# Performance work log

Measured on AMD Instinct MI355X. Metric: run time of the kernel, lower is better.

## Reference

```python
import jax, jax.numpy as jnp
import numpy as np

INPUT_DIM = 1024
EMBED_DIMS = 128


def setup_inputs() -> dict:
    key = jax.random.key(0)
    ks = jax.random.split(key, 7)
    s_in = 1.0 / np.sqrt(INPUT_DIM)
    x = jax.random.normal(ks[0], (4, 4096, INPUT_DIM), dtype=jnp.float32)
    Wq = jax.random.uniform(ks[1], (INPUT_DIM, EMBED_DIMS), jnp.float32, -s_in, s_in)
    bq = jax.random.uniform(ks[2], (EMBED_DIMS,), jnp.float32, -s_in, s_in)
    Wk = jax.random.uniform(ks[3], (INPUT_DIM, EMBED_DIMS), jnp.float32, -s_in, s_in)
    bk = jax.random.uniform(ks[4], (EMBED_DIMS,), jnp.float32, -s_in, s_in)
    Wv = jax.random.uniform(ks[5], (INPUT_DIM, EMBED_DIMS), jnp.float32, -s_in, s_in)
    bv = jax.random.uniform(ks[6], (EMBED_DIMS,), jnp.float32, -s_in, s_in)
    return {"x": x, "Wq": Wq, "bq": bq, "Wk": Wk, "bk": bk, "Wv": Wv, "bv": bv}


def reference(x, Wq, bq, Wk, bk, Wv, bv):
    # x: [B, L, C]
    Q = jnp.einsum('blc,cd->bld', x, Wq) + bq  # [B, L, D]
    K = jnp.einsum('blc,cd->bld', x, Wk) + bk
    V = jnp.einsum('blc,cd->bld', x, Wv) + bv
    d_k = Q.shape[-1]
    scores = jnp.einsum('bld,bmd->blm', Q, K) / jnp.sqrt(jnp.float32(d_k))  # [B, L, L]
    attn = jax.nn.softmax(scores, axis=-1)
    return jnp.einsum('blm,bmd->bld', attn, V)  # [B, L, D]
```

## Files before the change

### kernel.cpp

```cpp
#include <hip/hip_runtime.h>
#include <stdint.h>

typedef __bf16 bf16;
typedef __bf16 bf16x8 __attribute__((ext_vector_type(8)));
typedef __bf16 bf16x4 __attribute__((ext_vector_type(4)));
typedef _Float16 f16;
typedef f16 f16x8 __attribute__((ext_vector_type(8)));
typedef f16 f16x4 __attribute__((ext_vector_type(4)));
typedef float f32x16 __attribute__((ext_vector_type(16)));
typedef uint32_t u32x4 __attribute__((ext_vector_type(4)));

#define LQ    16384
#define CDIM  1024
#define DDIM  128
#define NSPLIT 4
#define QS 0.12751741f

static __device__ __forceinline__ uint32_t pkrtz(float a, float b) {
  return __builtin_bit_cast(uint32_t, __builtin_amdgcn_cvt_pkrtz(a, b));
}

static __device__ __forceinline__ void lds_barrier() {
  asm volatile("s_waitcnt lgkmcnt(0)" ::: "memory");
  __builtin_amdgcn_s_barrier();
}

static __device__ __forceinline__ void gload_lds16(const void* g, void* l) {
  __builtin_amdgcn_global_load_lds(
      (__attribute__((address_space(1))) void*)g,
      (__attribute__((address_space(3))) void*)l, 16, 0, 0);
}

__global__ void prep_kernel(const float* __restrict__ Wq, const float* __restrict__ Wk,
                            const float* __restrict__ Wv, const float* __restrict__ bq,
                            const float* __restrict__ bk, const float* __restrict__ bv,
                            bf16* __restrict__ Wt, float* __restrict__ bias_all) {
  int idx = blockIdx.x * 256 + threadIdx.x;
  int p = idx >> 17;
  int rem = idx & 131071;
  int k = rem >> 7, n = rem & 127;
  const float* W = (p == 0) ? Wq : (p == 1) ? Wk : Wv;
  float s = (p == 0) ? QS : 1.0f;
  Wt[(size_t)(p * 128 + n) * CDIM + k] = (bf16)(W[rem] * s);
  if (idx < 384) {
    int pp = idx >> 7, nn = idx & 127;
    const float* b = (pp == 0) ? bq : (pp == 1) ? bk : bv;
    bias_all[idx] = b[nn] * ((pp == 0) ? QS : 1.0f);
  }
}

__global__ __launch_bounds__(512, 1) void qkv_gemm(
    const float* __restrict__ x, const bf16* __restrict__ Wt,
    const float* __restrict__ bias_all,
    bf16* __restrict__ Qw, bf16* __restrict__ Kw, f16* __restrict__ Vtw) {
  __shared__ bf16 As[2][64 * 64];
  __shared__ bf16 Bs[2][384 * 64];
  const int t = threadIdx.x;
  const int w = t >> 6;
  const int lane = t & 63;
  const int l31 = lane & 31;
  const int hi = lane >> 5;
  const int m0 = blockIdx.x * 64;
  const int m_off = (w & 1) * 32;
  const int n_off = ((w >> 1) & 3) * 32;

  const f32x16 z16 = {0.f,0.f,0.f,0.f,0.f,0.f,0.f,0.f,0.f,0.f,0.f,0.f,0.f,0.f,0.f,0.f};
  f32x16 acc[3];
  acc[0] = z16; acc[1] = z16; acc[2] = z16;

  const int srow = t >> 3;
  const int g = t & 7;
  const int sgoff = (g ^ (srow & 7)) * 8;
  const int scol = g * 8;

  const int lrow = lane >> 3;
  const int lgr = (lane & 7) ^ lrow;
  const bf16* bsrc = Wt + (size_t)(w * 48 + lrow) * CDIM + lgr * 8;

  float4 xc0, xc1, xn0, xn1;

#pragma unroll
  for (int c = 0; c < 6; c++)
    gload_lds16(bsrc + (size_t)c * 8 * CDIM, &Bs[0][(w * 48 + c * 8) * 64]);
  {
    const float* p = &x[(size_t)(m0 + srow) * CDIM + scol];
    float4 a0 = *(const float4*)p;
    float4 a1 = *(const float4*)(p + 4);
    bf16x8 v;
    v[0] = (bf16)a0.x; v[1] = (bf16)a0.y; v[2] = (bf16)a0.z; v[3] = (bf16)a0.w;
    v[4] = (bf16)a1.x; v[5] = (bf16)a1.y; v[6] = (bf16)a1.z; v[7] = (bf16)a1.w;
    *(bf16x8*)&As[0][srow * 64 + sgoff] = v;
  }
  {
    const float* p = &x[(size_t)(m0 + srow) * CDIM + 64 + scol];
    xc0 = *(const float4*)p;
    xc1 = *(const float4*)(p + 4);
  }
  lds_barrier();

  for (int kc = 0; kc < 16; kc++) {
    bf16* Ab = As[kc & 1];
    bf16* Bb = Bs[kc & 1];

    if (kc < 15) {
      const bf16* s = bsrc + (kc + 1) * 64;
      bf16* Bn = Bs[(kc + 1) & 1];
#pragma unroll
      for (int c = 0; c < 6; c++)
        gload_lds16(s + (size_t)c * 8 * CDIM, &Bn[(w * 48 + c * 8) * 64]);
      __builtin_amdgcn_sched_barrier(0);
      if (kc < 14) {
        const float* p = &x[(size_t)(m0 + srow) * CDIM + (kc + 2) * 64 + scol];
        xn0 = *(const float4*)p;
        xn1 = *(const float4*)(p + 4);
      }
    }

#pragma unroll
    for (int ks = 0; ks < 4; ks++) {
      const int rg = ((ks * 2 + hi) ^ (l31 & 7)) * 8;
      bf16x8 af = *(const bf16x8*)&Ab[(m_off + l31) * 64 + rg];
#pragma unroll
      for (int p = 0; p < 3; p++) {
        bf16x8 bfr = *(const bf16x8*)&Bb[(p * 128 + n_off + l31) * 64 + rg];
        acc[p] = __builtin_amdgcn_mfma_f32_32x32x16_bf16(af, bfr, acc[p], 0, 0, 0);
      }
    }

    if (kc < 15) {
      bf16* An = As[(kc + 1) & 1];
      bf16x8 v;
      v[0] = (bf16)xc0.x; v[1] = (bf16)xc0.y; v[2] = (bf16)xc0.z; v[3] = (bf16)xc0.w;
      v[4] = (bf16)xc1.x; v[5] = (bf16)xc1.y; v[6] = (bf16)xc1.z; v[7] = (bf16)xc1.w;
      *(bf16x8*)&An[srow * 64 + sgoff] = v;
      __builtin_amdgcn_sched_barrier(0);
      if (kc < 14)
        asm volatile("s_waitcnt vmcnt(2)" ::: "memory");
      else
        asm volatile("s_waitcnt vmcnt(0)" ::: "memory");
      lds_barrier();
      xc0 = xn0; xc1 = xn1;
    }
  }

  const int n = n_off + l31;
#pragma unroll
  for (int p = 0; p < 3; p++) {
    const float bias = bias_all[p * 128 + n];
    if (p < 2) {
      bf16* outp = (p == 0) ? Qw : Kw;
#pragma unroll
      for (int r = 0; r < 16; r++) {
        int m = m0 + m_off + (r & 3) + 8 * (r >> 2) + 4 * hi;
        outp[(size_t)m * DDIM + n] = (bf16)(acc[p][r] + bias);
      }
    } else {
#pragma unroll
      for (int gq = 0; gq < 4; gq++) {
        int mbase = m0 + m_off + 8 * gq + 4 * hi;
        f16x4 pv;
#pragma unroll
        for (int r = 0; r < 4; r++) pv[r] = (f16)(acc[p][gq * 4 + r] + bias);
        *(f16x4*)&Vtw[(size_t)n * LQ + mbase] = pv;
      }
    }
  }
}

__global__ __launch_bounds__(256, 2) void flash_kernel(
    const bf16* __restrict__ Qw, const bf16* __restrict__ Kw, const f16* __restrict__ Vtw,
    bf16* __restrict__ Opb, float* __restrict__ lp) {
  __shared__ bf16 Kl[2][64 * 136];
  __shared__ f16  Vl[2][128 * 72];

  const int t = threadIdx.x;
  const int w = t >> 6;
  const int lane = t & 63;
  const int l31 = lane & 31;
  const int hi = lane >> 5;
  const int lin = blockIdx.y * 128 + blockIdx.x;
  const int logical = ((lin & 7) << 6) + (lin >> 3);
  const int qb = logical & 127;
  const int sp = logical >> 7;
  const int batch = qb >> 5;
  const int q0w = qb * 128 + w * 32;
  const int kv_base = batch * 4096 + sp * 1024;

  bf16x8 qf[8];
#pragma unroll
  for (int ks = 0; ks < 8; ks++)
    qf[ks] = *(const bf16x8*)&Qw[(size_t)(q0w + l31) * DDIM + ks * 16 + hi * 8];

  const f32x16 z16 = {0.f,0.f,0.f,0.f,0.f,0.f,0.f,0.f,0.f,0.f,0.f,0.f,0.f,0.f,0.f,0.f};
  f32x16 o[4];
  o[0] = z16; o[1] = z16; o[2] = z16; o[3] = z16;
  f32x16 liacc = z16;

  f16x8 ones;
#pragma unroll
  for (int i = 0; i < 8; i++) ones[i] = (f16)1.f;

  const int kr = t >> 4;
  const int kcol = (t & 15) << 3;
  const int vr = t >> 3;
  const int vcol = (t & 7) << 3;

  bf16x8 ka[4];
  f16x8 va[4];
  f16x8 pa[4];

#pragma unroll
  for (int c = 0; c < 4; c++)
    ka[c] = *(const bf16x8*)&Kw[(size_t)(kv_base + c * 16 + kr) * DDIM + kcol];
#pragma unroll
  for (int c = 0; c < 4; c++)
    va[c] = *(const f16x8*)&Vtw[(size_t)(c * 32 + vr) * LQ + kv_base + vcol];

#pragma unroll
  for (int c = 0; c < 4; c++)
    *(bf16x8*)&Kl[0][(c * 16 + kr) * 136 + kcol] = ka[c];
#pragma unroll
  for (int c = 0; c < 4; c++)
    *(f16x8*)&Vl[0][(c * 32 + vr) * 72 + vcol] = va[c];

#pragma unroll
  for (int c = 0; c < 4; c++)
    ka[c] = *(const bf16x8*)&Kw[(size_t)(kv_base + 64 + c * 16 + kr) * DDIM + kcol];
#pragma unroll
  for (int c = 0; c < 4; c++)
    va[c] = *(const f16x8*)&Vtw[(size_t)(c * 32 + vr) * LQ + kv_base + 64 + vcol];

  lds_barrier();

  f32x16 sv0 = z16, sv1 = z16;
  __builtin_amdgcn_s_setprio(1);
#pragma unroll
  for (int ks = 0; ks < 8; ks++) {
    bf16x8 kf0 = *(const bf16x8*)&Kl[0][l31 * 136 + ks * 16 + hi * 8];
    bf16x8 kf1 = *(const bf16x8*)&Kl[0][(32 + l31) * 136 + ks * 16 + hi * 8];
    sv0 = __builtin_amdgcn_mfma_f32_32x32x16_bf16(kf0, qf[ks], sv0, 0, 0, 0);
    sv1 = __builtin_amdgcn_mfma_f32_32x32x16_bf16(kf1, qf[ks], sv1, 0, 0, 0);
  }
  __builtin_amdgcn_s_setprio(0);
#pragma unroll
  for (int r = 0; r < 16; r++) {
    sv0[r] = __builtin_amdgcn_exp2f(sv0[r]);
    sv1[r] = __builtin_amdgcn_exp2f(sv1[r]);
  }
#pragma unroll
  for (int sl = 0; sl < 4; sl++) {
    const int b = (sl & 1) * 8;
    float s0 = (sl >> 1) ? sv1[b + 0] : sv0[b + 0];
    float s1 = (sl >> 1) ? sv1[b + 1] : sv0[b + 1];
    float s2 = (sl >> 1) ? sv1[b + 2] : sv0[b + 2];
    float s3 = (sl >> 1) ? sv1[b + 3] : sv0[b + 3];
    float s4 = (sl >> 1) ? sv1[b + 4] : sv0[b + 4];
    float s5 = (sl >> 1) ? sv1[b + 5] : sv0[b + 5];
    float s6 = (sl >> 1) ? sv1[b + 6] : sv0[b + 6];
    float s7 = (sl >> 1) ? sv1[b + 7] : sv0[b + 7];
    uint32_t a0 = pkrtz(s0, s1);
    uint32_t a1 = pkrtz(s2, s3);
    uint32_t a2 = pkrtz(s4, s5);
    uint32_t a3 = pkrtz(s6, s7);
    asm("v_permlane32_swap_b32 %0, %1" : "+v"(a0), "+v"(a2));
    asm("v_permlane32_swap_b32 %0, %1" : "+v"(a1), "+v"(a3));
    u32x4 aw; aw.x = a0; aw.y = a1; aw.z = a2; aw.w = a3;
    pa[sl] = __builtin_bit_cast(f16x8, aw);
  }

  for (int tile = 0; tile < 15; tile++) {
    bf16* Kb = Kl[(tile + 1) & 1];
    f16*  Vb = Vl[(tile + 1) & 1];
    f16*  Vp = Vl[tile & 1];
#pragma unroll
    for (int c = 0; c < 4; c++)
      *(bf16x8*)&Kb[(c * 16 + kr) * 136 + kcol] = ka[c];
#pragma unroll
    for (int c = 0; c < 4; c++)
      *(f16x8*)&Vb[(c * 32 + vr) * 72 + vcol] = va[c];

    const int kvn = kv_base + (tile < 14 ? tile + 2 : 15) * 64;
#pragma unroll
    for (int c = 0; c < 4; c++)
      ka[c] = *(const bf16x8*)&Kw[(size_t)(kvn + c * 16 + kr) * DDIM + kcol];
#pragma unroll
    for (int c = 0; c < 4; c++)
      va[c] = *(const f16x8*)&Vtw[(size_t)(c * 32 + vr) * LQ + kvn + vcol];

    lds_barrier();

    sv0 = z16; sv1 = z16;
    __builtin_amdgcn_s_setprio(1);
#pragma unroll
    for (int i = 0; i < 4; i++) {
      bf16x8 kf0a = *(const bf16x8*)&Kb[l31 * 136 + (2 * i) * 16 + hi * 8];
      bf16x8 kf1a = *(const bf16x8*)&Kb[(32 + l31) * 136 + (2 * i) * 16 + hi * 8];
      bf16x8 kf0b = *(const bf16x8*)&Kb[l31 * 136 + (2 * i + 1) * 16 + hi * 8];
      bf16x8 kf1b = *(const bf16x8*)&Kb[(32 + l31) * 136 + (2 * i + 1) * 16 + hi * 8];
      sv0 = __builtin_amdgcn_mfma_f32_32x32x16_bf16(kf0a, qf[2 * i], sv0, 0, 0, 0);
      sv1 = __builtin_amdgcn_mfma_f32_32x32x16_bf16(kf1a, qf[2 * i], sv1, 0, 0, 0);
      const int koff = (i >> 1) * 32 + (i & 1) * 16 + hi * 8;
#pragma unroll
      for (int dt = 0; dt < 4; dt++) {
        f16x8 vf = *(const f16x8*)&Vp[(dt * 32 + l31) * 72 + koff];
        o[dt] = __builtin_amdgcn_mfma_f32_32x32x16_f16(pa[i], vf, o[dt], 0, 0, 0);
      }
      liacc = __builtin_amdgcn_mfma_f32_32x32x16_f16(pa[i], ones, liacc, 0, 0, 0);
      sv0 = __builtin_amdgcn_mfma_f32_32x32x16_bf16(kf0b, qf[2 * i + 1], sv0, 0, 0, 0);
      sv1 = __builtin_amdgcn_mfma_f32_32x32x16_bf16(kf1b, qf[2 * i + 1], sv1, 0, 0, 0);
    }
    __builtin_amdgcn_s_setprio(0);

#pragma unroll
    for (int r = 0; r < 16; r++) {
      sv0[r] = __builtin_amdgcn_exp2f(sv0[r]);
      sv1[r] = __builtin_amdgcn_exp2f(sv1[r]);
    }
#pragma unroll
    for (int sl = 0; sl < 4; sl++) {
      const int b = (sl & 1) * 8;
      float s0 = (sl >> 1) ? sv1[b + 0] : sv0[b + 0];
      float s1 = (sl >> 1) ? sv1[b + 1] : sv0[b + 1];
      float s2 = (sl >> 1) ? sv1[b + 2] : sv0[b + 2];
      float s3 = (sl >> 1) ? sv1[b + 3] : sv0[b + 3];
      float s4 = (sl >> 1) ? sv1[b + 4] : sv0[b + 4];
      float s5 = (sl >> 1) ? sv1[b + 5] : sv0[b + 5];
      float s6 = (sl >> 1) ? sv1[b + 6] : sv0[b + 6];
      float s7 = (sl >> 1) ? sv1[b + 7] : sv0[b + 7];
      uint32_t a0 = pkrtz(s0, s1);
      uint32_t a1 = pkrtz(s2, s3);
      uint32_t a2 = pkrtz(s4, s5);
      uint32_t a3 = pkrtz(s6, s7);
      asm("v_permlane32_swap_b32 %0, %1" : "+v"(a0), "+v"(a2));
      asm("v_permlane32_swap_b32 %0, %1" : "+v"(a1), "+v"(a3));
      u32x4 aw; aw.x = a0; aw.y = a1; aw.z = a2; aw.w = a3;
      pa[sl] = __builtin_bit_cast(f16x8, aw);
    }

    __builtin_amdgcn_s_barrier();
  }

  {
    f16* Vp = Vl[15 & 1];
    __builtin_amdgcn_s_setprio(1);
#pragma unroll
    for (int i = 0; i < 4; i++) {
      const int koff = (i >> 1) * 32 + (i & 1) * 16 + hi * 8;
#pragma unroll
      for (int dt = 0; dt < 4; dt++) {
        f16x8 vf = *(const f16x8*)&Vp[(dt * 32 + l31) * 72 + koff];
        o[dt] = __builtin_amdgcn_mfma_f32_32x32x16_f16(pa[i], vf, o[dt], 0, 0, 0);
      }
      liacc = __builtin_amdgcn_mfma_f32_32x32x16_f16(pa[i], ones, liacc, 0, 0, 0);
    }
    __builtin_amdgcn_s_setprio(0);
  }

  const size_t po = (size_t)sp * LQ * DDIM;
#pragma unroll
  for (int dt = 0; dt < 4; dt++)
#pragma unroll
    for (int r = 0; r < 16; r++) {
      int q = q0w + (r & 3) + 8 * (r >> 2) + 4 * hi;
      Opb[po + (size_t)q * DDIM + dt * 32 + l31] = (bf16)o[dt][r];
    }
  if (l31 == 0) {
#pragma unroll
    for (int r = 0; r < 16; r++)
      lp[(size_t)sp * LQ + q0w + (r & 3) + 8 * (r >> 2) + 4 * hi] = liacc[r];
  }
}

__global__ void combine_kernel(const bf16* __restrict__ Opb, const float* __restrict__ lp,
                               float* __restrict__ out) {
  int idx = blockIdx.x * 256 + threadIdx.x;
  int q = idx >> 5;
  int d = (idx & 31) * 4;
  float lsum = 0.f;
  float acc[4] = {0.f, 0.f, 0.f, 0.f};
#pragma unroll
  for (int sp = 0; sp < NSPLIT; sp++) {
    lsum += lp[(size_t)sp * LQ + q];
    bf16x4 ov = *(const bf16x4*)&Opb[(size_t)sp * LQ * DDIM + (size_t)q * DDIM + d];
#pragma unroll
    for (int j = 0; j < 4; j++) acc[j] += (float)ov[j];
  }
  float inv = 1.0f / lsum;
  float4 r;
  r.x = acc[0] * inv; r.y = acc[1] * inv; r.z = acc[2] * inv; r.w = acc[3] * inv;
  *(float4*)&out[(size_t)q * DDIM + d] = r;
}

extern "C" void kernel_launch(void* const* d_in, const int* in_sizes, int n_in,
                              void* d_out, int out_size, void* d_ws, size_t ws_size,
                              hipStream_t stream) {
  const float* x  = (const float*)d_in[0];
  const float* Wq = (const float*)d_in[1];
  const float* bq = (const float*)d_in[2];
  const float* Wk = (const float*)d_in[3];
  const float* bk = (const float*)d_in[4];
  const float* Wv = (const float*)d_in[5];
  const float* bv = (const float*)d_in[6];
  char* ws = (char*)d_ws;
  bf16* Qw   = (bf16*)(ws);
  bf16* Kw   = (bf16*)(ws + ((size_t)4 << 20));
  f16*  Vtw  = (f16*)(ws + ((size_t)8 << 20));
  bf16* Wt   = (bf16*)(ws + ((size_t)12 << 20));
  float* bias_all = (float*)(ws + ((size_t)12 << 20) + 786432);
  bf16* Opb  = (bf16*)(ws + ((size_t)13 << 20));
  float* lpp = (float*)(ws + ((size_t)29 << 20));
  float* out = (float*)d_out;

  prep_kernel<<<1536, 256, 0, stream>>>(Wq, Wk, Wv, bq, bk, bv, Wt, bias_all);
  qkv_gemm<<<256, 512, 0, stream>>>(x, Wt, bias_all, Qw, Kw, Vtw);
  flash_kernel<<<dim3(128, NSPLIT), 256, 0, stream>>>(Qw, Kw, Vtw, Opb, lpp);
  combine_kernel<<<2048, 256, 0, stream>>>(Opb, lpp, out);
}
```

Measured before the change: 167.3 us.

## Process 64 query rows per wave in flash kernel to reuse K/V fragments

Each wave now handles two 32-row query tiles instead of one. Every K and V fragment read from LDS therefore feeds twice as many MFMAs, and the grid shrinks from 512 to 256 blocks, each covering 256 queries. Launch bounds drop to one block per SIMD-set to leave room for the doubled accumulators. The cost is much higher register pressure and lower occupancy, with 256 blocks on a 256-CU device giving only one wave of blocks and less latency hiding.

```diff
diff --git a/kernel.cpp b/kernel.cpp
--- a/kernel.cpp
+++ b/kernel.cpp
@@ -167,7 +167,7 @@
   }
 }
 
-__global__ __launch_bounds__(256, 2) void flash_kernel(
+__global__ __launch_bounds__(256, 1) void flash_kernel(
     const bf16* __restrict__ Qw, const bf16* __restrict__ Kw, const f16* __restrict__ Vtw,
     bf16* __restrict__ Opb, float* __restrict__ lp) {
   __shared__ bf16 Kl[2][64 * 136];
@@ -178,23 +178,26 @@
   const int lane = t & 63;
   const int l31 = lane & 31;
   const int hi = lane >> 5;
-  const int lin = blockIdx.y * 128 + blockIdx.x;
-  const int logical = ((lin & 7) << 6) + (lin >> 3);
-  const int qb = logical & 127;
-  const int sp = logical >> 7;
-  const int batch = qb >> 5;
-  const int q0w = qb * 128 + w * 32;
+  const int lin = blockIdx.y * 64 + blockIdx.x;
+  const int logical = ((lin & 7) << 5) + (lin >> 3);
+  const int qb = logical & 63;
+  const int sp = logical >> 6;
+  const int batch = qb >> 4;
+  const int q0w = qb * 256 + w * 64;
   const int kv_base = batch * 4096 + sp * 1024;
 
-  bf16x8 qf[8];
-#pragma unroll
-  for (int ks = 0; ks < 8; ks++)
-    qf[ks] = *(const bf16x8*)&Qw[(size_t)(q0w + l31) * DDIM + ks * 16 + hi * 8];
+  bf16x8 qf0[8], qf1[8];
+#pragma unroll
+  for (int ks = 0; ks < 8; ks++) {
+    qf0[ks] = *(const bf16x8*)&Qw[(size_t)(q0w + l31) * DDIM + ks * 16 + hi * 8];
+    qf1[ks] = *(const bf16x8*)&Qw[(size_t)(q0w + 32 + l31) * DDIM + ks * 16 + hi * 8];
+  }
 
   const f32x16 z16 = {0.f,0.f,0.f,0.f,0.f,0.f,0.f,0.f,0.f,0.f,0.f,0.f,0.f,0.f,0.f,0.f};
-  f32x16 o[4];
-  o[0] = z16; o[1] = z16; o[2] = z16; o[3] = z16;
-  f32x16 liacc = z16;
+  f32x16 o0[4], o1[4];
+#pragma unroll
+  for (int dt = 0; dt < 4; dt++) { o0[dt] = z16; o1[dt] = z16; }
+  f32x16 li0 = z16, li1 = z16;
 
   f16x8 ones;
 #pragma unroll
@@ -207,7 +210,7 @@
 
   bf16x8 ka[4];
   f16x8 va[4];
-  f16x8 pa[4];
+  f16x8 pa0[4], pa1[4];
 
 #pragma unroll
   for (int c = 0; c < 4; c++)
@@ -232,40 +235,50 @@
 
   lds_barrier();
 
-  f32x16 sv0 = z16, sv1 = z16;
+  f32x16 s00 = z16, s01 = z16, s10 = z16, s11 = z16;
   __builtin_amdgcn_s_setprio(1);
 #pragma unroll
   for (int ks = 0; ks < 8; ks++) {
     bf16x8 kf0 = *(const bf16x8*)&Kl[0][l31 * 136 + ks * 16 + hi * 8];
     bf16x8 kf1 = *(const bf16x8*)&Kl[0][(32 + l31) * 136 + ks * 16 + hi * 8];
-    sv0 = __builtin_amdgcn_mfma_f32_32x32x16_bf16(kf0, qf[ks], sv0, 0, 0, 0);
-    sv1 = __builtin_amdgcn_mfma_f32_32x32x16_bf16(kf1, qf[ks], sv1, 0, 0, 0);
+    s00 = __builtin_amdgcn_mfma_f32_32x32x16_bf16(kf0, qf0[ks], s00, 0, 0, 0);
+    s01 = __builtin_amdgcn_mfma_f32_32x32x16_bf16(kf0, qf1[ks], s01, 0, 0, 0);
+    s10 = __builtin_amdgcn_mfma_f32_32x32x16_bf16(kf1, qf0[ks], s10, 0, 0, 0);
+    s11 = __builtin_amdgcn_mfma_f32_32x32x16_bf16(kf1, qf1[ks], s11, 0, 0, 0);
   }
   __builtin_amdgcn_s_setprio(0);
 #pragma unroll
   for (int r = 0; r < 16; r++) {
-    sv0[r] = __builtin_amdgcn_exp2f(sv0[r]);
-    sv1[r] = __builtin_amdgcn_exp2f(sv1[r]);
+    s00[r] = __builtin_amdgcn_exp2f(s00[r]);
+    s01[r] = __builtin_amdgcn_exp2f(s01[r]);
+    s10[r] = __builtin_amdgcn_exp2f(s10[r]);
+    s11[r] = __builtin_amdgcn_exp2f(s11[r]);
   }
 #pragma unroll
   for (int sl = 0; sl < 4; sl++) {
     const int b = (sl & 1) * 8;
-    float s0 = (sl >> 1) ? sv1[b + 0] : sv0[b + 0];
-    float s1 = (sl >> 1) ? sv1[b + 1] : sv0[b + 1];
-    float s2 = (sl >> 1) ? sv1[b + 2] : sv0[b + 2];
-    float s3 = (sl >> 1) ? sv1[b + 3] : sv0[b + 3];
-    float s4 = (sl >> 1) ? sv1[b + 4] : sv0[b + 4];
-    float s5 = (sl >> 1) ? sv1[b + 5] : sv0[b + 5];
-    float s6 = (sl >> 1) ? sv1[b + 6] : sv0[b + 6];
-    float s7 = (sl >> 1) ? sv1[b + 7] : sv0[b + 7];
-    uint32_t a0 = pkrtz(s0, s1);
-    uint32_t a1 = pkrtz(s2, s3);
-    uint32_t a2 = pkrtz(s4, s5);
-    uint32_t a3 = pkrtz(s6, s7);
-    asm("v_permlane32_swap_b32 %0, %1" : "+v"(a0), "+v"(a2));
-    asm("v_permlane32_swap_b32 %0, %1" : "+v"(a1), "+v"(a3));
-    u32x4 aw; aw.x = a0; aw.y = a1; aw.z = a2; aw.w = a3;
-    pa[sl] = __builtin_bit_cast(f16x8, aw);
+    {
+      const f32x16 s = (sl >> 1) ? s10 : s00;
+      uint32_t a0 = pkrtz(s[b + 0], s[b + 1]);
+      uint32_t a1 = pkrtz(s[b + 2], s[b + 3]);
+      uint32_t a2 = pkrtz(s[b + 4], s[b + 5]);
+      uint32_t a3 = pkrtz(s[b + 6], s[b + 7]);
+      asm("v_permlane32_swap_b32 %0, %1" : "+v"(a0), "+v"(a2));
+      asm("v_permlane32_swap_b32 %0, %1" : "+v"(a1), "+v"(a3));
+      u32x4 aw; aw.x = a0; aw.y = a1; aw.z = a2; aw.w = a3;
+      pa0[sl] = __builtin_bit_cast(f16x8, aw);
+    }
+    {
+      const f32x16 s = (sl >> 1) ? s11 : s01;
+      uint32_t a0 = pkrtz(s[b + 0], s[b + 1]);
+      uint32_t a1 = pkrtz(s[b + 2], s[b + 3]);
+      uint32_t a2 = pkrtz(s[b + 4], s[b + 5]);
+      uint32_t a3 = pkrtz(s[b + 6], s[b + 7]);
+      asm("v_permlane32_swap_b32 %0, %1" : "+v"(a0), "+v"(a2));
+      asm("v_permlane32_swap_b32 %0, %1" : "+v"(a1), "+v"(a3));
+      u32x4 aw; aw.x = a0; aw.y = a1; aw.z = a2; aw.w = a3;
+      pa1[sl] = __builtin_bit_cast(f16x8, aw);
+    }
   }
 
   for (int tile = 0; tile < 15; tile++) {
@@ -289,7 +302,7 @@
 
     lds_barrier();
 
-    sv0 = z16; sv1 = z16;
+    s00 = z16; s01 = z16; s10 = z16; s11 = z16;
     __builtin_amdgcn_s_setprio(1);
 #pragma unroll
     for (int i = 0; i < 4; i++) {
@@ -297,44 +310,58 @@
       bf16x8 kf1a = *(const bf16x8*)&Kb[(32 + l31) * 136 + (2 * i) * 16 + hi * 8];
       bf16x8 kf0b = *(const bf16x8*)&Kb[l31 * 136 + (2 * i + 1) * 16 + hi * 8];
       bf16x8 kf1b = *(const bf16x8*)&Kb[(32 + l31) * 136 + (2 * i + 1) * 16 + hi * 8];
-      sv0 = __builtin_amdgcn_mfma_f32_32x32x16_bf16(kf0a, qf[2 * i], sv0, 0, 0, 0);
-      sv1 = __builtin_amdgcn_mfma_f32_32x32x16_bf16(kf1a, qf[2 * i], sv1, 0, 0, 0);
+      s00 = __builtin_amdgcn_mfma_f32_32x32x16_bf16(kf0a, qf0[2 * i], s00, 0, 0, 0);
+      s01 = __builtin_amdgcn_mfma_f32_32x32x16_bf16(kf0a, qf1[2 * i], s01, 0, 0, 0);
+      s10 = __builtin_amdgcn_mfma_f32_32x32x16_bf16(kf1a, qf0[2 * i], s10, 0, 0, 0);
+      s11 = __builtin_amdgcn_mfma_f32_32x32x16_bf16(kf1a, qf1[2 * i], s11, 0, 0, 0);
       const int koff = (i >> 1) * 32 + (i & 1) * 16 + hi * 8;
 #pragma unroll
       for (int dt = 0; dt < 4; dt++) {
         f16x8 vf = *(const f16x8*)&Vp[(dt * 32 + l31) * 72 + koff];
-        o[dt] = __builtin_amdgcn_mfma_f32_32x32x16_f16(pa[i], vf, o[dt], 0, 0, 0);
-      }
-      liacc = __builtin_amdgcn_mfma_f32_32x32x16_f16(pa[i], ones, liacc, 0, 0, 0);
-      sv0 = __builtin_amdgcn_mfma_f32_32x32x16_bf16(kf0b, qf[2 * i + 1], sv0, 0, 0, 0);
-      sv1 = __builtin_amdgcn_mfma_f32_32x32x16_bf16(kf1b, qf[2 * i + 1], sv1, 0, 0, 0);
+        o0[dt] = __builtin_amdgcn_mfma_f32_32x32x16_f16(pa0[i], vf, o0[dt], 0, 0, 0);
+        o1[dt] = __builtin_amdgcn_mfma_f32_32x32x16_f16(pa1[i], vf, o1[dt], 0, 0, 0);
+      }
+      li0 = __builtin_amdgcn_mfma_f32_32x32x16_f16(pa0[i], ones, li0, 0, 0, 0);
+      li1 = __builtin_amdgcn_mfma_f32_32x32x16_f16(pa1[i], ones, li1, 0, 0, 0);
+      s00 = __builtin_amdgcn_mfma_f32_32x32x16_bf16(kf0b, qf0[2 * i + 1], s00, 0, 0, 0);
+      s01 = __builtin_amdgcn_mfma_f32_32x32x16_bf16(kf0b, qf1[2 * i + 1], s01, 0, 0, 0);
+      s10 = __builtin_amdgcn_mfma_f32_32x32x16_bf16(kf1b, qf0[2 * i + 1], s10, 0, 0, 0);
+      s11 = __builtin_amdgcn_mfma_f32_32x32x16_bf16(kf1b, qf1[2 * i + 1], s11, 0, 0, 0);
     }
     __builtin_amdgcn_s_setprio(0);
 
 #pragma unroll
     for (int r = 0; r < 16; r++) {
-      sv0[r] = __builtin_amdgcn_exp2f(sv0[r]);
-      sv1[r] = __builtin_amdgcn_exp2f(sv1[r]);
+      s00[r] = __builtin_amdgcn_exp2f(s00[r]);
+      s01[r] = __builtin_amdgcn_exp2f(s01[r]);
+      s10[r] = __builtin_amdgcn_exp2f(s10[r]);
+      s11[r] = __builtin_amdgcn_exp2f(s11[r]);
     }
 #pragma unroll
     for (int sl = 0; sl < 4; sl++) {
       const int b = (sl & 1) * 8;
-      float s0 = (sl >> 1) ? sv1[b + 0] : sv0[b + 0];
-      float s1 = (sl >> 1) ? sv1[b + 1] : sv0[b + 1];
-      float s2 = (sl >> 1) ? sv1[b + 2] : sv0[b + 2];
-      float s3 = (sl >> 1) ? sv1[b + 3] : sv0[b + 3];
-      float s4 = (sl >> 1) ? sv1[b + 4] : sv0[b + 4];
-      float s5 = (sl >> 1) ? sv1[b + 5] : sv0[b + 5];
-      float s6 = (sl >> 1) ? sv1[b + 6] : sv0[b + 6];
-      float s7 = (sl >> 1) ? sv1[b + 7] : sv0[b + 7];
-      uint32_t a0 = pkrtz(s0, s1);
-      uint32_t a1 = pkrtz(s2, s3);
-      uint32_t a2 = pkrtz(s4, s5);
-      uint32_t a3 = pkrtz(s6, s7);
-      asm("v_permlane32_swap_b32 %0, %1" : "+v"(a0), "+v"(a2));
-      asm("v_permlane32_swap_b32 %0, %1" : "+v"(a1), "+v"(a3));
-      u32x4 aw; aw.x = a0; aw.y = a1; aw.z = a2; aw.w = a3;
-      pa[sl] = __builtin_bit_cast(f16x8, aw);
+      {
+        const f32x16 s = (sl >> 1) ? s10 : s00;
+        uint32_t a0 = pkrtz(s[b + 0], s[b + 1]);
+        uint32_t a1 = pkrtz(s[b + 2], s[b + 3]);
+        uint32_t a2 = pkrtz(s[b + 4], s[b + 5]);
+        uint32_t a3 = pkrtz(s[b + 6], s[b + 7]);
+        asm("v_permlane32_swap_b32 %0, %1" : "+v"(a0), "+v"(a2));
+        asm("v_permlane32_swap_b32 %0, %1" : "+v"(a1), "+v"(a3));
+        u32x4 aw; aw.x = a0; aw.y = a1; aw.z = a2; aw.w = a3;
+        pa0[sl] = __builtin_bit_cast(f16x8, aw);
+      }
+      {
+        const f32x16 s = (sl >> 1) ? s11 : s01;
+        uint32_t a0 = pkrtz(s[b + 0], s[b + 1]);
+        uint32_t a1 = pkrtz(s[b + 2], s[b + 3]);
+        uint32_t a2 = pkrtz(s[b + 4], s[b + 5]);
+        uint32_t a3 = pkrtz(s[b + 6], s[b + 7]);
+        asm("v_permlane32_swap_b32 %0, %1" : "+v"(a0), "+v"(a2));
+        asm("v_permlane32_swap_b32 %0, %1" : "+v"(a1), "+v"(a3));
+        u32x4 aw; aw.x = a0; aw.y = a1; aw.z = a2; aw.w = a3;
+        pa1[sl] = __builtin_bit_cast(f16x8, aw);
+      }
     }
 
     __builtin_amdgcn_s_barrier();
@@ -349,9 +376,11 @@
 #pragma unroll
       for (int dt = 0; dt < 4; dt++) {
         f16x8 vf = *(const f16x8*)&Vp[(dt * 32 + l31) * 72 + koff];
-        o[dt] = __builtin_amdgcn_mfma_f32_32x32x16_f16(pa[i], vf, o[dt], 0, 0, 0);
-      }
-      liacc = __builtin_amdgcn_mfma_f32_32x32x16_f16(pa[i], ones, liacc, 0, 0, 0);
+        o0[dt] = __builtin_amdgcn_mfma_f32_32x32x16_f16(pa0[i], vf, o0[dt], 0, 0, 0);
+        o1[dt] = __builtin_amdgcn_mfma_f32_32x32x16_f16(pa1[i], vf, o1[dt], 0, 0, 0);
+      }
+      li0 = __builtin_amdgcn_mfma_f32_32x32x16_f16(pa0[i], ones, li0, 0, 0, 0);
+      li1 = __builtin_amdgcn_mfma_f32_32x32x16_f16(pa1[i], ones, li1, 0, 0, 0);
     }
     __builtin_amdgcn_s_setprio(0);
   }
@@ -361,13 +390,17 @@
   for (int dt = 0; dt < 4; dt++)
 #pragma unroll
     for (int r = 0; r < 16; r++) {
-      int q = q0w + (r & 3) + 8 * (r >> 2) + 4 * hi;
-      Opb[po + (size_t)q * DDIM + dt * 32 + l31] = (bf16)o[dt][r];
+      int crow = (r & 3) + 8 * (r >> 2) + 4 * hi;
+      Opb[po + (size_t)(q0w + crow) * DDIM + dt * 32 + l31] = (bf16)o0[dt][r];
+      Opb[po + (size_t)(q0w + 32 + crow) * DDIM + dt * 32 + l31] = (bf16)o1[dt][r];
     }
   if (l31 == 0) {
 #pragma unroll
-    for (int r = 0; r < 16; r++)
-      lp[(size_t)sp * LQ + q0w + (r & 3) + 8 * (r >> 2) + 4 * hi] = liacc[r];
+    for (int r = 0; r < 16; r++) {
+      int crow = (r & 3) + 8 * (r >> 2) + 4 * hi;
+      lp[(size_t)sp * LQ + q0w + crow] = li0[r];
+      lp[(size_t)sp * LQ + q0w + 32 + crow] = li1[r];
+    }
   }
 }
 
@@ -413,6 +446,6 @@
 
   prep_kernel<<<1536, 256, 0, stream>>>(Wq, Wk, Wv, bq, bk, bv, Wt, bias_all);
   qkv_gemm<<<256, 512, 0, stream>>>(x, Wt, bias_all, Qw, Kw, Vtw);
-  flash_kernel<<<dim3(128, NSPLIT), 256, 0, stream>>>(Qw, Kw, Vtw, Opb, lpp);
+  flash_kernel<<<dim3(64, NSPLIT), 256, 0, stream>>>(Qw, Kw, Vtw, Opb, lpp);
   combine_kernel<<<2048, 256, 0, stream>>>(Opb, lpp, out);
 }
```

Result: slower. 172.4 us (+3.1%).
